# Performance work log

Hardware: AMD Instinct MI355X
Metric: run time of the kernel (lower is better)

Reference implementation:

```python
import jax, jax.numpy as jnp
import numpy as np
import math

B, T, C = 4, 2048, 1024
NH, D = 16, 64


def setup_inputs() -> dict:
    key = jax.random.key(0)
    ks = jax.random.split(key, 7)
    s = 0.02
    return {
        "x": jax.random.normal(ks[0], (B, T, C), dtype=jnp.float32),
        "W_attn": jax.random.normal(ks[1], (C, 3 * C), dtype=jnp.float32) * s,
        "b_attn": jax.random.normal(ks[2], (3 * C,), dtype=jnp.float32) * s,
        "W_proj": jax.random.normal(ks[3], (C, C), dtype=jnp.float32) * s,
        "b_proj": jax.random.normal(ks[4], (C,), dtype=jnp.float32) * s,
        # bQ/bK emulate mean_Q + std_Q*randn (resampled biases), broadcast over heads
        "bQ": 0.5 + 0.1 * jax.random.normal(ks[5], (NH, D), dtype=jnp.float32),
        "bK": 0.3 + 0.1 * jax.random.normal(ks[6], (NH, D), dtype=jnp.float32),
    }


def reference(x, W_attn, b_attn, W_proj, b_proj, bQ, bK):
    b, t, c = x.shape
    nh, d = bQ.shape
    qkv = x @ W_attn + b_attn                       # [B,T,3C]
    q, k, v = jnp.split(qkv, 3, axis=2)
    # [B,T,C] -> [B,nh,T,d]
    q = q.reshape(b, t, nh, d).transpose(0, 2, 1, 3)
    k = k.reshape(b, t, nh, d).transpose(0, 2, 1, 3)
    v = v.reshape(b, t, nh, d).transpose(0, 2, 1, 3)
    q = q + bQ[None, :, None, :]
    k = k + bK[None, :, None, :]
    scores = jnp.einsum('bhqd,bhkd->bhqk', q, k) / math.sqrt(d)
    causal = jnp.tril(jnp.ones((t, t), dtype=bool))
    scores = jnp.where(causal[None, None], scores, jnp.finfo(scores.dtype).min)
    att = jax.nn.softmax(scores, axis=-1)
    y = jnp.einsum('bhqk,bhkd->bhqd', att, v)       # [B,nh,T,d]
    y = y.transpose(0, 2, 1, 3).reshape(b, t, c)
    out = y @ W_proj + b_proj
    return (out, bQ)
```

## Files before the change

### kernel.cpp

```cpp
#include <hip/hip_runtime.h>
#include <hip/hip_bf16.h>

#define B_  4
#define T_  2048
#define C_  1024
#define NH_ 16
#define D_  64
#define BH_ (B_*NH_)
#define M_  (B_*T_)

typedef __attribute__((ext_vector_type(8))) short short8;
typedef __attribute__((ext_vector_type(4))) short short4v;
typedef __attribute__((ext_vector_type(4))) float f32x4;

#define SC2 0.18033688011112043f

__device__ __forceinline__ ushort f2bf(float f) {
    unsigned u = __float_as_uint(f);
    u += 0x7FFF + ((u >> 16) & 1);
    return (ushort)(u >> 16);
}

__device__ __forceinline__ unsigned cvtpk(float lo, float hi) {
    unsigned r;
    asm("v_cvt_pk_bf16_f32 %0, %1, %2" : "=v"(r) : "v"(lo), "v"(hi));
    return r;
}

__device__ __forceinline__ void gload16(const void* g, void* lds) {
    __builtin_amdgcn_global_load_lds(
        (const __attribute__((address_space(1))) void*)g,
        (__attribute__((address_space(3))) void*)lds, 16, 0, 0);
}

__global__ __launch_bounds__(256) void prepass_kernel(
    const float* __restrict__ x, ushort* __restrict__ Xb,
    const float* __restrict__ Wa, ushort* __restrict__ Wat,
    const float* __restrict__ bQ, float* __restrict__ bqDst)
{
    __shared__ float t[64][65];
    const int bid = blockIdx.x;
    const int tid = threadIdx.x;

    if (bid < 2048) {
        const int n8 = M_*C_/8;
        const int stride = 2048 * 256;
        for (int idx = bid*256 + tid; idx < n8; idx += stride) {
            const float* p = x + (size_t)idx * 8;
            f32x4 a = *(const f32x4*)p;
            f32x4 b = *(const f32x4*)(p + 4);
            union { short8 v; ushort u[8]; } pk;
            #pragma unroll
            for (int j = 0; j < 4; ++j) { pk.u[j] = f2bf(a[j]); pk.u[4+j] = f2bf(b[j]); }
            *(short8*)&Xb[(size_t)idx * 8] = pk.v;
        }
    } else if (bid < 2816) {
        const int tb = bid - 2048;
        const int n0 = (tb % 48) * 64;
        const int k0 = (tb / 48) * 64;
        const int K = C_, N = 3*C_;
        #pragma unroll
        for (int it = 0; it < 16; ++it) {
            const int kr = it*4 + (tid >> 6);
            t[kr][tid & 63] = Wa[(size_t)(k0 + kr) * N + n0 + (tid & 63)];
        }
        __syncthreads();
        const int nr8 = tid >> 3;
        const int kc0 = (tid & 7) * 8;
        #pragma unroll
        for (int j = 0; j < 2; ++j) {
            const int nr = j*32 + nr8;
            union { short8 v; ushort u[8]; } pk;
            #pragma unroll
            for (int e = 0; e < 8; ++e) pk.u[e] = f2bf(t[kc0 + e][nr]);
            *(short8*)&Wat[(size_t)(n0 + nr) * K + k0 + kc0] = pk.v;
        }
    } else {
        for (int i = tid; i < NH_*D_; i += 256) bqDst[i] = bQ[i];
    }
}

__global__ __launch_bounds__(256) void transpose_w_kernel(
    const float* __restrict__ in, ushort* __restrict__ out, int K, int N)
{
    __shared__ float t[64][65];
    const int tid = threadIdx.x;
    const int n0 = blockIdx.x * 64;
    const int k0 = blockIdx.y * 64;
    #pragma unroll
    for (int it = 0; it < 16; ++it) {
        const int kr = it*4 + (tid >> 6);
        t[kr][tid & 63] = in[(size_t)(k0 + kr) * N + n0 + (tid & 63)];
    }
    __syncthreads();
    const int nr8 = tid >> 3;
    const int kc0 = (tid & 7) * 8;
    #pragma unroll
    for (int j = 0; j < 2; ++j) {
        const int nr = j*32 + nr8;
        union { short8 v; ushort u[8]; } pk;
        #pragma unroll
        for (int e = 0; e < 8; ++e) pk.u[e] = f2bf(t[kc0 + e][nr]);
        *(short8*)&out[(size_t)(n0 + nr) * K + k0 + kc0] = pk.v;
    }
}

__global__ __launch_bounds__(512) void gemmqkv_kernel(
    const ushort* __restrict__ A, const ushort* __restrict__ Bt,
    const float* __restrict__ b_attn, const float* __restrict__ bQv,
    const float* __restrict__ bKv,
    ushort* __restrict__ Qb, ushort* __restrict__ Kb, ushort* __restrict__ Vt)
{
    __shared__ ushort SH[36864];

    const int K = C_;
    const int tid  = threadIdx.x;
    const int lane = tid & 63;
    const int w    = tid >> 6;
    const int wr   = w >> 2;
    const int wc   = w & 3;
    const int l16  = lane & 15, lg = lane >> 4;

    const int bid = blockIdx.x;
    const int xcd = bid & 7;
    const int idx = bid >> 3;
    const int m0  = (xcd*8 + (idx & 7)) * 128;
    const int n0  = (idx >> 3) * 256;

    const ushort* aBase = A  + (size_t)(m0 + w*16 + (lane >> 2)) * K + (lane & 3)*8;
    const ushort* bBase = Bt + (size_t)(n0 + w*32 + (lane >> 2)) * K + (lane & 3)*8;

    f32x4 acc[4][4] = {};
    const int NT = K >> 5;

    #define STAGE(tk, bi)                                                     \
        do {                                                                  \
            const size_t kn_ = (size_t)(tk) * 32;                             \
            gload16(aBase + kn_,               SH + (bi)*4096 + w*512);       \
            gload16(bBase + kn_,               SH + 12288 + (bi)*8192 + w*1024); \
            gload16(bBase + (size_t)16*K + kn_,SH + 12288 + (bi)*8192 + w*1024 + 512); \
        } while (0)

    STAGE(0, 0);
    STAGE(1, 1);
    asm volatile("s_waitcnt vmcnt(3)" ::: "memory");
    __builtin_amdgcn_s_barrier();

    #pragma unroll 1
    for (int t = 0; t < NT; ++t) {
        const int cur = t % 3;
        if (t + 2 < NT)
            STAGE(t + 2, (t + 2) % 3);

        short8 af[4], bf[4];
        #pragma unroll
        for (int i = 0; i < 4; ++i) {
            af[i] = *(const short8*)&SH[cur*4096 + (wr*64 + i*16 + l16)*32 + lg*8];
            bf[i] = *(const short8*)&SH[12288 + cur*8192 + (wc*64 + i*16 + l16)*32 + lg*8];
        }
        #pragma unroll
        for (int mi = 0; mi < 4; ++mi)
            #pragma unroll
            for (int ni = 0; ni < 4; ++ni)
                acc[mi][ni] = __builtin_amdgcn_mfma_f32_16x16x32_bf16(
                    af[mi], bf[ni], acc[mi][ni], 0, 0, 0);

        if (t + 1 < NT) {
            if (t + 2 < NT)
                asm volatile("s_waitcnt vmcnt(3)" ::: "memory");
            else
                asm volatile("s_waitcnt vmcnt(0)" ::: "memory");
            __builtin_amdgcn_s_barrier();
        }
    }
    #undef STAGE

    if (n0 < 2048) {
        #pragma unroll
        for (int ni = 0; ni < 4; ++ni) {
            const int n = n0 + wc*64 + ni*16 + l16;
            const int sec = n >> 10;
            const int nn  = n & 1023;
            const int h = nn >> 6, d = nn & 63;
            const float ba = b_attn[n];
            #pragma unroll
            for (int mi = 0; mi < 4; ++mi) {
                #pragma unroll
                for (int r = 0; r < 4; ++r) {
                    const int m = m0 + wr*64 + mi*16 + lg*4 + r;
                    const int b = m >> 11, tt = m & 2047;
                    float v = acc[mi][ni][r] + ba;
                    if (sec == 0) {
                        v = (v + bQv[nn]) * SC2;
                        Qb[((size_t)(b*NH_ + h)*T_ + tt)*D_ + d] = f2bf(v);
                    } else {
                        v += bKv[nn];
                        Kb[((size_t)(b*NH_ + h)*T_ + tt)*D_ + d] = f2bf(v);
                    }
                }
            }
        }
    } else {
        __syncthreads();
        ushort* TL = SH;
        const int bblk  = m0 >> 11;
        const int tcol0 = m0 & 2047;
        const int h0    = (n0 & 1023) >> 6;
        #pragma unroll
        for (int ni = 0; ni < 4; ++ni) {
            const int nl = wc*64 + ni*16 + l16;
            const float ba = b_attn[n0 + nl];
            #pragma unroll
            for (int mi = 0; mi < 4; ++mi)
                #pragma unroll
                for (int r = 0; r < 4; ++r)
                    TL[nl*136 + wr*64 + mi*16 + lg*4 + r] =
                        f2bf(acc[mi][ni][r] + ba);
        }
        __syncthreads();
        #pragma unroll
        for (int it = 0; it < 4; ++it) {
            const int row  = it*64 + (tid >> 3);
            const int slot = tid & 7;
            const int d = row & 63, h = h0 + (row >> 6);
            ushort* dst = Vt + ((size_t)(bblk*NH_ + h)*D_ + d)*T_
                          + tcol0 + slot*16;
            *(short8*)dst       = *(const short8*)&TL[row*136 + slot*16];
            *(short8*)(dst + 8) = *(const short8*)&TL[row*136 + slot*16 + 8];
        }
    }
}

__global__ __launch_bounds__(256) void gemm2_kernel(
    const ushort* __restrict__ A, const ushort* __restrict__ Bt,
    float* __restrict__ outp, const float* __restrict__ b_proj,
    int K, int N)
{
    __shared__ ushort SH[24576];

    const int tid  = threadIdx.x;
    const int lane = tid & 63;
    const int w    = tid >> 6;
    const int wr   = w >> 1, wc = w & 1;
    const int l16  = lane & 15, lg = lane >> 4;

    const int bid = blockIdx.x;
    const int xcd = bid & 7;
    const int idx = bid >> 3;
    const int m0  = (xcd*8 + (idx & 7)) * 128;
    const int n0  = (idx >> 3) * 128;

    const int srow = lane >> 2;
    const int scol = (lane & 3) * 8;
    const ushort* aS = A  + (size_t)(m0 + w*32 + srow) * K + scol;
    const ushort* bS = Bt + (size_t)(n0 + w*32 + srow) * K + scol;

    f32x4 acc[4][4] = {};
    const int NT = K >> 5;

    #define STAGE(tk, bi)                                                     \
        do {                                                                  \
            const int kn_ = (tk) * 32;                                        \
            gload16(aS + kn_,                SH + (bi)*4096 + w*1024);        \
            gload16(aS + (size_t)16*K + kn_, SH + (bi)*4096 + w*1024 + 512);  \
            gload16(bS + kn_,                SH + 12288 + (bi)*4096 + w*1024);\
            gload16(bS + (size_t)16*K + kn_, SH + 12288 + (bi)*4096 + w*1024 + 512);\
        } while (0)

    STAGE(0, 0);
    STAGE(1, 1);
    asm volatile("s_waitcnt vmcnt(4)" ::: "memory");
    __builtin_amdgcn_s_barrier();

    for (int t = 0; t < NT; ++t) {
        const int cur = t % 3;
        if (t + 2 < NT)
            STAGE(t + 2, (t + 2) % 3);

        short8 af[4], bf[4];
        #pragma unroll
        for (int i = 0; i < 4; ++i) {
            af[i] = *(const short8*)&SH[cur*4096 + (wr*64 + i*16 + l16)*32 + lg*8];
            bf[i] = *(const short8*)&SH[12288 + cur*4096 + (wc*64 + i*16 + l16)*32 + lg*8];
        }
        #pragma unroll
        for (int mi = 0; mi < 4; ++mi)
            #pragma unroll
            for (int ni = 0; ni < 4; ++ni)
                acc[mi][ni] = __builtin_amdgcn_mfma_f32_16x16x32_bf16(
                    af[mi], bf[ni], acc[mi][ni], 0, 0, 0);

        if (t + 1 < NT) {
            if (t + 2 < NT)
                asm volatile("s_waitcnt vmcnt(4)" ::: "memory");
            else
                asm volatile("s_waitcnt vmcnt(0)" ::: "memory");
            __builtin_amdgcn_s_barrier();
        }
    }
    #undef STAGE

    #pragma unroll
    for (int ni = 0; ni < 4; ++ni) {
        const int n = n0 + wc*64 + ni*16 + l16;
        const float bp = b_proj[n];
        #pragma unroll
        for (int mi = 0; mi < 4; ++mi)
            #pragma unroll
            for (int r = 0; r < 4; ++r) {
                const int m = m0 + wr*64 + mi*16 + lg*4 + r;
                outp[(size_t)m * N + n] = acc[mi][ni][r] + bp;
            }
    }
}

__global__ __launch_bounds__(256, 5) void attn_kernel(
    const ushort* __restrict__ Qb, const ushort* __restrict__ Kb,
    const ushort* __restrict__ Vt, ushort* __restrict__ y)
{
    __shared__ char lds[2][16384];

    const int tid  = threadIdx.x;
    const int lane = tid & 63;
    const int w    = tid >> 6;
    const int l16  = lane & 15, lg = lane >> 4;
    const int bid  = blockIdx.x;
    const int xcd  = bid & 7;
    const int idx  = bid >> 3;
    const int bh   = (xcd << 3) | (idx & 7);
    const int p    = 31 - (idx >> 3);
    const int b    = bh >> 4, h = bh & 15;
    const size_t kvb = (size_t)bh * T_ * D_;
    const size_t vtb = (size_t)bh * D_ * T_;

    int srow[2], scol[2];
    #pragma unroll
    for (int i = 0; i < 2; ++i) {
        const int l = w*2048 + i*1024 + lane*16;
        const int r = l >> 7;
        const int c = (l & 127) ^ ((r & 7) << 4);
        srow[i] = r; scol[i] = c >> 1;
    }

    const f32x4 minit = {-14.f, -14.f, -14.f, -14.f};

    const int qw = p * 64 + w * 16;

    short8 qf[2];
    #pragma unroll
    for (int c = 0; c < 2; ++c)
        qf[c] = *(const short8*)(Qb + kvb +
                    (size_t)(qw + l16)*D_ + c*32 + lg*8);

    f32x4 o[4] = {};
    float lrow = 0.f;
    const int nt = p + 1;

    #pragma unroll
    for (int i = 0; i < 2; ++i) {
        gload16(Kb + kvb + (size_t)srow[i]*D_ + scol[i],
                &lds[0][w*2048 + i*1024]);
        gload16(Vt + vtb + (size_t)srow[i]*T_ + scol[i],
                &lds[0][8192 + w*2048 + i*1024]);
    }

    #pragma unroll 1
    for (int t = 0; t < nt; ++t) {
        const int kb = t * 64;
        if (t + 1 < nt) {
            char* Lb = lds[(t + 1) & 1];
            const int kb1 = kb + 64;
            #pragma unroll
            for (int i = 0; i < 2; ++i) {
                gload16(Kb + kvb + (size_t)(kb1 + srow[i])*D_ + scol[i],
                        Lb + w*2048 + i*1024);
                gload16(Vt + vtb + (size_t)srow[i]*T_ + kb1 + scol[i],
                        Lb + 8192 + w*2048 + i*1024);
            }
            asm volatile("s_waitcnt vmcnt(4)" ::: "memory");
        } else {
            asm volatile("s_waitcnt vmcnt(0)" ::: "memory");
        }
        __builtin_amdgcn_s_barrier();

        {
            const char* Lk = lds[t & 1];
            const char* Lv = lds[t & 1] + 8192;

            f32x4 s[4];
            #pragma unroll
            for (int t4 = 0; t4 < 4; ++t4) {
                const int r = t4*16 + l16;
                const int m = (r & 7) << 4;
                const short8 kc0 = *(const short8*)(Lk + r*128 + (( lg*16     ) ^ m));
                const short8 kc1 = *(const short8*)(Lk + r*128 + ((64 + lg*16 ) ^ m));
                s[t4] = __builtin_amdgcn_mfma_f32_16x16x32_bf16(kc0, qf[0], minit, 0, 0, 0);
                s[t4] = __builtin_amdgcn_mfma_f32_16x16x32_bf16(kc1, qf[1], s[t4], 0, 0, 0);
            }

            const bool full = (kb + 63 <= qw);
            float x[4][4];
            float rs = 0.f;
            #pragma unroll
            for (int t4 = 0; t4 < 4; ++t4)
                #pragma unroll
                for (int r = 0; r < 4; ++r) {
                    float v = s[t4][r];
                    if (!full)
                        v = (kb + t4*16 + lg*4 + r <= qw + l16) ? v : -1e30f;
                    const float pe = __builtin_amdgcn_exp2f(v);
                    x[t4][r] = pe;
                    rs += pe;
                }
            rs += __shfl_xor(rs, 16, 64);
            rs += __shfl_xor(rs, 32, 64);
            lrow += rs;

            union { unsigned u[4]; short8 v; } p0, p1;
            p0.u[0] = cvtpk(x[0][0], x[0][1]);
            p0.u[1] = cvtpk(x[0][2], x[0][3]);
            p0.u[2] = cvtpk(x[1][0], x[1][1]);
            p0.u[3] = cvtpk(x[1][2], x[1][3]);
            p1.u[0] = cvtpk(x[2][0], x[2][1]);
            p1.u[1] = cvtpk(x[2][2], x[2][3]);
            p1.u[2] = cvtpk(x[3][0], x[3][1]);
            p1.u[3] = cvtpk(x[3][2], x[3][3]);

            #pragma unroll
            for (int cb = 0; cb < 4; ++cb) {
                const int d = cb*16 + l16;
                const int mv = (d & 7) << 4;
                const char* vb = Lv + d*128;
                union { short8 v; short4v hh[2]; } v0, v1;
                v0.hh[0] = *(const short4v*)(vb + ((lg*8     ) ^ mv));
                v0.hh[1] = *(const short4v*)(vb + ((lg*8 + 32) ^ mv));
                v1.hh[0] = *(const short4v*)(vb + ((lg*8 + 64) ^ mv));
                v1.hh[1] = *(const short4v*)(vb + ((lg*8 + 96) ^ mv));
                o[cb] = __builtin_amdgcn_mfma_f32_16x16x32_bf16(v0.v, p0.v, o[cb], 0, 0, 0);
                o[cb] = __builtin_amdgcn_mfma_f32_16x16x32_bf16(v1.v, p1.v, o[cb], 0, 0, 0);
            }
        }
        __builtin_amdgcn_s_barrier();
    }

    {
        const float inv = 1.0f / lrow;
        const int q = qw + l16;
        ushort* yr = y + ((size_t)b*T_ + q)*C_ + h*D_ + lg*4;
        #pragma unroll
        for (int cb = 0; cb < 4; ++cb) {
            union { unsigned u[2]; short4v v; } st;
            st.u[0] = cvtpk(o[cb][0]*inv, o[cb][1]*inv);
            st.u[1] = cvtpk(o[cb][2]*inv, o[cb][3]*inv);
            *(short4v*)(yr + cb*16) = st.v;
        }
    }
}

extern "C" void kernel_launch(void* const* d_in, const int* in_sizes, int n_in,
                              void* d_out, int out_size, void* d_ws, size_t ws_size,
                              hipStream_t stream)
{
    const float* x      = (const float*)d_in[0];
    const float* W_attn = (const float*)d_in[1];
    const float* b_attn = (const float*)d_in[2];
    const float* W_proj = (const float*)d_in[3];
    const float* b_proj = (const float*)d_in[4];
    const float* bQ     = (const float*)d_in[5];
    const float* bK     = (const float*)d_in[6];
    float* out = (float*)d_out;

    const size_t HE = (size_t)BH_ * T_ * D_;
    ushort* Qb = (ushort*)d_ws;
    ushort* Kb = Qb + HE;
    ushort* Vt = Kb + HE;
    ushort* y  = Vt + HE;
    ushort* Wpt = (ushort*)d_ws;

    ushort* Xb  = (ushort*)d_out;
    ushort* Wat = (ushort*)d_out + (size_t)M_ * C_;

    prepass_kernel<<<2817, 256, 0, stream>>>(x, Xb, W_attn, Wat,
                                             bQ, out + (size_t)M_ * C_);

    gemmqkv_kernel<<<768, 512, 0, stream>>>(
        Xb, Wat, b_attn, bQ, bK, Qb, Kb, Vt);

    attn_kernel<<<2048, 256, 0, stream>>>(Qb, Kb, Vt, y);

    transpose_w_kernel<<<dim3(C_/64, C_/64), 256, 0, stream>>>(W_proj, Wpt, C_, C_);

    gemm2_kernel<<<512, 256, 0, stream>>>(
        y, Wpt, out, b_proj, C_, C_);
}
```

Baseline: 175.2 us.

## Process 128-query tiles per attention block to reuse K/V loads

Each attention block now handles 128 queries (two 16-row groups per wave) instead of 64, halving the grid and reusing every K/V tile loaded into LDS for twice as many queries. Waves skip compute on tiles past their causal limit but still join the barriers. The cost is more registers per thread, since the launch-bounds occupancy hint is dropped, and coarser causal load balance with fewer blocks.

```diff
diff --git a/kernel.cpp b/kernel.cpp
--- a/kernel.cpp
+++ b/kernel.cpp
@@ -314,7 +314,7 @@
     }
 }
 
-__global__ __launch_bounds__(256, 5) void attn_kernel(
+__global__ __launch_bounds__(256) void attn_kernel(
     const ushort* __restrict__ Qb, const ushort* __restrict__ Kb,
     const ushort* __restrict__ Vt, ushort* __restrict__ y)
 {
@@ -328,7 +328,7 @@
     const int xcd  = bid & 7;
     const int idx  = bid >> 3;
     const int bh   = (xcd << 3) | (idx & 7);
-    const int p    = 31 - (idx >> 3);
+    const int p    = 15 - (idx >> 3);
     const int b    = bh >> 4, h = bh & 15;
     const size_t kvb = (size_t)bh * T_ * D_;
     const size_t vtb = (size_t)bh * D_ * T_;
@@ -344,17 +344,19 @@
 
     const f32x4 minit = {-14.f, -14.f, -14.f, -14.f};
 
-    const int qw = p * 64 + w * 16;
-
-    short8 qf[2];
-    #pragma unroll
-    for (int c = 0; c < 2; ++c)
-        qf[c] = *(const short8*)(Qb + kvb +
-                    (size_t)(qw + l16)*D_ + c*32 + lg*8);
-
-    f32x4 o[4] = {};
-    float lrow = 0.f;
-    const int nt = p + 1;
+    const int qw = p * 128 + w * 32;
+
+    short8 qf[2][2];
+    #pragma unroll
+    for (int g = 0; g < 2; ++g)
+        #pragma unroll
+        for (int c = 0; c < 2; ++c)
+            qf[g][c] = *(const short8*)(Qb + kvb +
+                        (size_t)(qw + g*16 + l16)*D_ + c*32 + lg*8);
+
+    f32x4 o[2][4] = {};
+    float lrow[2] = {0.f, 0.f};
+    const int nt = 2*p + 2;
 
     #pragma unroll
     for (int i = 0; i < 2; ++i) {
@@ -383,48 +385,54 @@
         }
         __builtin_amdgcn_s_barrier();
 
-        {
+        if (kb <= qw + 31) {
             const char* Lk = lds[t & 1];
             const char* Lv = lds[t & 1] + 8192;
 
-            f32x4 s[4];
+            f32x4 s[2][4];
             #pragma unroll
             for (int t4 = 0; t4 < 4; ++t4) {
                 const int r = t4*16 + l16;
                 const int m = (r & 7) << 4;
                 const short8 kc0 = *(const short8*)(Lk + r*128 + (( lg*16     ) ^ m));
                 const short8 kc1 = *(const short8*)(Lk + r*128 + ((64 + lg*16 ) ^ m));
-                s[t4] = __builtin_amdgcn_mfma_f32_16x16x32_bf16(kc0, qf[0], minit, 0, 0, 0);
-                s[t4] = __builtin_amdgcn_mfma_f32_16x16x32_bf16(kc1, qf[1], s[t4], 0, 0, 0);
+                s[0][t4] = __builtin_amdgcn_mfma_f32_16x16x32_bf16(kc0, qf[0][0], minit,    0, 0, 0);
+                s[0][t4] = __builtin_amdgcn_mfma_f32_16x16x32_bf16(kc1, qf[0][1], s[0][t4], 0, 0, 0);
+                s[1][t4] = __builtin_amdgcn_mfma_f32_16x16x32_bf16(kc0, qf[1][0], minit,    0, 0, 0);
+                s[1][t4] = __builtin_amdgcn_mfma_f32_16x16x32_bf16(kc1, qf[1][1], s[1][t4], 0, 0, 0);
             }
 
-            const bool full = (kb + 63 <= qw);
-            float x[4][4];
-            float rs = 0.f;
-            #pragma unroll
-            for (int t4 = 0; t4 < 4; ++t4)
+            union { unsigned u[4]; short8 v; } pk[2][2];
+            #pragma unroll
+            for (int g = 0; g < 2; ++g) {
+                const int qlo = qw + g*16;
+                const bool full = (kb + 63 <= qlo);
+                float x[4][4];
+                float rs = 0.f;
                 #pragma unroll
-                for (int r = 0; r < 4; ++r) {
-                    float v = s[t4][r];
-                    if (!full)
-                        v = (kb + t4*16 + lg*4 + r <= qw + l16) ? v : -1e30f;
-                    const float pe = __builtin_amdgcn_exp2f(v);
-                    x[t4][r] = pe;
-                    rs += pe;
-                }
-            rs += __shfl_xor(rs, 16, 64);
-            rs += __shfl_xor(rs, 32, 64);
-            lrow += rs;
-
-            union { unsigned u[4]; short8 v; } p0, p1;
-            p0.u[0] = cvtpk(x[0][0], x[0][1]);
-            p0.u[1] = cvtpk(x[0][2], x[0][3]);
-            p0.u[2] = cvtpk(x[1][0], x[1][1]);
-            p0.u[3] = cvtpk(x[1][2], x[1][3]);
-            p1.u[0] = cvtpk(x[2][0], x[2][1]);
-            p1.u[1] = cvtpk(x[2][2], x[2][3]);
-            p1.u[2] = cvtpk(x[3][0], x[3][1]);
-            p1.u[3] = cvtpk(x[3][2], x[3][3]);
+                for (int t4 = 0; t4 < 4; ++t4)
+                    #pragma unroll
+                    for (int r = 0; r < 4; ++r) {
+                        float v = s[g][t4][r];
+                        if (!full)
+                            v = (kb + t4*16 + lg*4 + r <= qlo + l16) ? v : -1e30f;
+                        const float pe = __builtin_amdgcn_exp2f(v);
+                        x[t4][r] = pe;
+                        rs += pe;
+                    }
+                rs += __shfl_xor(rs, 16, 64);
+                rs += __shfl_xor(rs, 32, 64);
+                lrow[g] += rs;
+
+                pk[g][0].u[0] = cvtpk(x[0][0], x[0][1]);
+                pk[g][0].u[1] = cvtpk(x[0][2], x[0][3]);
+                pk[g][0].u[2] = cvtpk(x[1][0], x[1][1]);
+                pk[g][0].u[3] = cvtpk(x[1][2], x[1][3]);
+                pk[g][1].u[0] = cvtpk(x[2][0], x[2][1]);
+                pk[g][1].u[1] = cvtpk(x[2][2], x[2][3]);
+                pk[g][1].u[2] = cvtpk(x[3][0], x[3][1]);
+                pk[g][1].u[3] = cvtpk(x[3][2], x[3][3]);
+            }
 
             #pragma unroll
             for (int cb = 0; cb < 4; ++cb) {
@@ -436,22 +444,25 @@
                 v0.hh[1] = *(const short4v*)(vb + ((lg*8 + 32) ^ mv));
                 v1.hh[0] = *(const short4v*)(vb + ((lg*8 + 64) ^ mv));
                 v1.hh[1] = *(const short4v*)(vb + ((lg*8 + 96) ^ mv));
-                o[cb] = __builtin_amdgcn_mfma_f32_16x16x32_bf16(v0.v, p0.v, o[cb], 0, 0, 0);
-                o[cb] = __builtin_amdgcn_mfma_f32_16x16x32_bf16(v1.v, p1.v, o[cb], 0, 0, 0);
+                o[0][cb] = __builtin_amdgcn_mfma_f32_16x16x32_bf16(v0.v, pk[0][0].v, o[0][cb], 0, 0, 0);
+                o[0][cb] = __builtin_amdgcn_mfma_f32_16x16x32_bf16(v1.v, pk[0][1].v, o[0][cb], 0, 0, 0);
+                o[1][cb] = __builtin_amdgcn_mfma_f32_16x16x32_bf16(v0.v, pk[1][0].v, o[1][cb], 0, 0, 0);
+                o[1][cb] = __builtin_amdgcn_mfma_f32_16x16x32_bf16(v1.v, pk[1][1].v, o[1][cb], 0, 0, 0);
             }
         }
         __builtin_amdgcn_s_barrier();
     }
 
-    {
-        const float inv = 1.0f / lrow;
-        const int q = qw + l16;
+    #pragma unroll
+    for (int g = 0; g < 2; ++g) {
+        const float inv = 1.0f / lrow[g];
+        const int q = qw + g*16 + l16;
         ushort* yr = y + ((size_t)b*T_ + q)*C_ + h*D_ + lg*4;
         #pragma unroll
         for (int cb = 0; cb < 4; ++cb) {
             union { unsigned u[2]; short4v v; } st;
-            st.u[0] = cvtpk(o[cb][0]*inv, o[cb][1]*inv);
-            st.u[1] = cvtpk(o[cb][2]*inv, o[cb][3]*inv);
+            st.u[0] = cvtpk(o[g][cb][0]*inv, o[g][cb][1]*inv);
+            st.u[1] = cvtpk(o[g][cb][2]*inv, o[g][cb][3]*inv);
             *(short4v*)(yr + cb*16) = st.v;
         }
     }
@@ -486,7 +497,7 @@
     gemmqkv_kernel<<<768, 512, 0, stream>>>(
         Xb, Wat, b_attn, bQ, bK, Qb, Kb, Vt);
 
-    attn_kernel<<<2048, 256, 0, stream>>>(Qb, Kb, Vt, y);
+    attn_kernel<<<1024, 256, 0, stream>>>(Qb, Kb, Vt, y);
 
     transpose_w_kernel<<<dim3(C_/64, C_/64), 256, 0, stream>>>(W_proj, Wpt, C_, C_);
 
```

Measured after the change: 177.2 us. Within noise of the previous version (+1.2%).

## Pair causal query tiles in 512-thread attention blocks to share K/V loads

Applied to the files above, without the earlier changes.

The attention kernel now launches 1024 blocks of 512 threads. Each block holds two query super-tiles, pp and 31-pp, that share the same K/V stream, so each block does the same number of iterations and the K/V tile staged in LDS is reused by both. Warps whose query tile is already past the current key tile skip the compute but still join the barriers. This is meant to balance the causal triangle and halve global K/V traffic per query, at the cost of idle warps in the short half and lower occupancy per CU from the larger blocks.

```diff
diff --git a/kernel.cpp b/kernel.cpp
--- a/kernel.cpp
+++ b/kernel.cpp
@@ -314,7 +314,7 @@
     }
 }
 
-__global__ __launch_bounds__(256, 5) void attn_kernel(
+__global__ __launch_bounds__(512) void attn_kernel(
     const ushort* __restrict__ Qb, const ushort* __restrict__ Kb,
     const ushort* __restrict__ Vt, ushort* __restrict__ y)
 {
@@ -328,23 +328,21 @@
     const int xcd  = bid & 7;
     const int idx  = bid >> 3;
     const int bh   = (xcd << 3) | (idx & 7);
-    const int p    = 31 - (idx >> 3);
+    const int pp   = idx >> 3;
     const int b    = bh >> 4, h = bh & 15;
     const size_t kvb = (size_t)bh * T_ * D_;
     const size_t vtb = (size_t)bh * D_ * T_;
 
-    int srow[2], scol[2];
-    #pragma unroll
-    for (int i = 0; i < 2; ++i) {
-        const int l = w*2048 + i*1024 + lane*16;
-        const int r = l >> 7;
-        const int c = (l & 127) ^ ((r & 7) << 4);
-        srow[i] = r; scol[i] = c >> 1;
-    }
+    const int sl   = w*1024 + lane*16;
+    const int srow = sl >> 7;
+    const int scol = ((sl & 127) ^ ((srow & 7) << 4)) >> 1;
 
     const f32x4 minit = {-14.f, -14.f, -14.f, -14.f};
 
-    const int qw = p * 64 + w * 16;
+    const int grp  = w >> 2;
+    const int qsup = grp ? pp : (31 - pp);
+    const int qw   = qsup*64 + (w & 3)*16;
+    const int nt   = 32 - pp;
 
     short8 qf[2];
     #pragma unroll
@@ -354,15 +352,9 @@
 
     f32x4 o[4] = {};
     float lrow = 0.f;
-    const int nt = p + 1;
-
-    #pragma unroll
-    for (int i = 0; i < 2; ++i) {
-        gload16(Kb + kvb + (size_t)srow[i]*D_ + scol[i],
-                &lds[0][w*2048 + i*1024]);
-        gload16(Vt + vtb + (size_t)srow[i]*T_ + scol[i],
-                &lds[0][8192 + w*2048 + i*1024]);
-    }
+
+    gload16(Kb + kvb + (size_t)srow*D_ + scol, &lds[0][w*1024]);
+    gload16(Vt + vtb + (size_t)srow*T_ + scol, &lds[0][8192 + w*1024]);
 
     #pragma unroll 1
     for (int t = 0; t < nt; ++t) {
@@ -370,20 +362,15 @@
         if (t + 1 < nt) {
             char* Lb = lds[(t + 1) & 1];
             const int kb1 = kb + 64;
-            #pragma unroll
-            for (int i = 0; i < 2; ++i) {
-                gload16(Kb + kvb + (size_t)(kb1 + srow[i])*D_ + scol[i],
-                        Lb + w*2048 + i*1024);
-                gload16(Vt + vtb + (size_t)srow[i]*T_ + kb1 + scol[i],
-                        Lb + 8192 + w*2048 + i*1024);
-            }
-            asm volatile("s_waitcnt vmcnt(4)" ::: "memory");
+            gload16(Kb + kvb + (size_t)(kb1 + srow)*D_ + scol, Lb + w*1024);
+            gload16(Vt + vtb + (size_t)srow*T_ + kb1 + scol,  Lb + 8192 + w*1024);
+            asm volatile("s_waitcnt vmcnt(2)" ::: "memory");
         } else {
             asm volatile("s_waitcnt vmcnt(0)" ::: "memory");
         }
         __builtin_amdgcn_s_barrier();
 
-        {
+        if (kb <= qw + 15) {
             const char* Lk = lds[t & 1];
             const char* Lv = lds[t & 1] + 8192;
 
@@ -486,7 +473,7 @@
     gemmqkv_kernel<<<768, 512, 0, stream>>>(
         Xb, Wat, b_attn, bQ, bK, Qb, Kb, Vt);
 
-    attn_kernel<<<2048, 256, 0, stream>>>(Qb, Kb, Vt, y);
+    attn_kernel<<<1024, 512, 0, stream>>>(Qb, Kb, Vt, y);
 
     transpose_w_kernel<<<dim3(C_/64, C_/64), 256, 0, stream>>>(W_proj, Wpt, C_, C_);
 
```

Result: slower. 180.2 us (+2.9%).
